# Kernel optimization log

Hardware: AMD Instinct MI355X
Metric: run time of the kernel (lower is better)

The kernel has to match this reference:

```python
import jax, jax.numpy as jnp
import numpy as np

PUSH_MARGIN = 0.25


def setup_inputs() -> dict:
    key = jax.random.key(0)
    k1, k2 = jax.random.split(key)
    B, H, W, D, K = 8, 512, 512, 32, 64
    embeddings = jax.random.normal(k1, (B, H, W, D), dtype=jnp.float32)
    labels = jax.random.randint(k2, (B, H, W), 0, K, dtype=jnp.int32)
    return {"embeddings": embeddings, "labels": labels, "n_instances": K}


def _metric_loss(embeddings, labels, n_instances):
    # embeddings: (B, H, W, D) float; labels: (B, H, W) int; n_instances: static int K
    B = embeddings.shape[0]
    D = embeddings.shape[-1]
    K = n_instances
    emb = embeddings.reshape(B, -1, D)          # (B, N, D)
    lab = labels.reshape(B, -1).astype(jnp.int32)  # (B, N)

    # One-pass segment reduce over all batches: offset labels per batch element.
    seg = (lab + jnp.arange(B, dtype=jnp.int32)[:, None] * K).reshape(-1)  # (B*N,)
    sums = jax.ops.segment_sum(emb.reshape(-1, D), seg, num_segments=B * K)
    counts = jax.ops.segment_sum(jnp.ones(seg.shape, dtype=emb.dtype), seg,
                                 num_segments=B * K)
    sums = sums.reshape(B, K, D)
    counts = counts.reshape(B, K)
    present = counts > 0.5                       # non-empty instances (B, K)
    centroids = sums / jnp.maximum(counts, 1.0)[..., None]  # (B, K, D); zeros if empty

    # Pairwise Manhattan distances between centroids: (B, K, K)
    dist = jnp.sum(jnp.abs(centroids[:, :, None, :] - centroids[:, None, :, :]), axis=-1)
    hinge = jax.nn.relu(PUSH_MARGIN - dist)      # push: relu(margin - d)
    sq = hinge * hinge                           # squared error metric

    # strictly upper triangular + only pairs of non-empty instances
    triu = jnp.triu(jnp.ones((K, K), dtype=bool), k=1)
    pair_mask = triu[None] & present[:, :, None] & present[:, None, :]
    per_image_sum = jnp.sum(jnp.where(pair_mask, sq, 0.0), axis=(1, 2))  # (B,)

    n = jnp.sum(present.astype(emb.dtype), axis=1)              # (B,) non-empty count
    n_comparisons = n * (n - 1.0) / 2.0
    push_loss = per_image_sum / n_comparisons
    return jnp.mean(push_loss)


def reference(embeddings, labels, n_instances):
    return _metric_loss(embeddings, labels, n_instances)
```

## Files before the change

kernel.cpp:

```cpp
#include <hip/hip_runtime.h>

#define B_    8
#define N_    (512 * 512)
#define D_    32
#define K_    64
#define TPB   256
#define NWAVE (TPB / 64)
#define KROW  36
#define TABW  (K_ * KROW)
#define REC   (K_ * D_ + K_)
#define RECQ  (REC / 4)

#define PROC(LB, V, PBASE)                                                    \
  {                                                                           \
    const int    lbc = LB;                                                    \
    const float4 vc  = V;                                                     \
    const int    pb  = (PBASE);                                               \
    if (pb < iend) {                                      \
      LB = lab[bbase + pb + eg];                                              \
      V  = embv[(bbase + pb + eg) * 8 + d4];                                  \
    }                                                                         \
    claimv[lbc] = egl;                           \
    const int win = (claimv[lbc] == egl);             \
    if (d4 == 0) atomicAdd(&cnt[lbc], 1.0f);            \
    const int a = lbc * KROW + d4 * 4;                                        \
    if (win) {                                                                \
      float4 cur = *reinterpret_cast<const float4*>(tab + a);                 \
      cur.x += vc.x; cur.y += vc.y; cur.z += vc.z; cur.w += vc.w;             \
      *reinterpret_cast<float4*>(tab + a) = cur;                              \
    } else {         \
      atomicAdd(&tab[a + 0], vc.x);                                           \
      atomicAdd(&tab[a + 1], vc.y);                                           \
      atomicAdd(&tab[a + 2], vc.z);                                           \
      atomicAdd(&tab[a + 3], vc.w);                                           \
    }                                                                         \
  }

__global__ __launch_bounds__(TPB) void seg_partial_kernel(
    const float* __restrict__ emb, const int* __restrict__ lab,
    float* __restrict__ partials, int blk_per_b)
{
    __shared__ __align__(16) float s_tab[NWAVE * TABW];
    __shared__ float s_cnt[NWAVE * K_];
    __shared__ int   s_claim[NWAVE * K_];

    for (int i = threadIdx.x; i < NWAVE * TABW; i += TPB) s_tab[i] = 0.f;
    for (int i = threadIdx.x; i < NWAVE * K_;  i += TPB) s_cnt[i] = 0.f;
    __syncthreads();

    const int tid  = threadIdx.x;
    const int wave = tid >> 6;
    const int lane = tid & 63;
    const int egl  = lane >> 3;
    const int d4   = lane & 7;
    const int eg   = wave * 8 + egl;

    float* __restrict__ tab = s_tab + wave * TABW;
    float* __restrict__ cnt = s_cnt + wave * K_;
    volatile int* claimv = s_claim + wave * K_;

    const int blk = blockIdx.x;
    const int b   = blk / blk_per_b;
    const int bib = blk - b * blk_per_b;
    const long long bbase = (long long)b * N_;
    const float4* __restrict__ embv = reinterpret_cast<const float4*>(emb);
    const int CHUNK = N_ / blk_per_b;
    int ib = bib * CHUNK;
    const int iend = ib + CHUNK;

    int lbA = lab[bbase + ib + eg];
    float4 vA = embv[(bbase + ib + eg) * 8 + d4];
    int lbB = 0;
    float4 vB = make_float4(0.f, 0.f, 0.f, 0.f);
    if (ib + 32 < iend) {
        lbB = lab[bbase + ib + 32 + eg];
        vB  = embv[(bbase + ib + 32 + eg) * 8 + d4];
    }

    for (;;) {
        PROC(lbA, vA, ib + 64);
        ib += 32;
        if (ib >= iend) break;
        PROC(lbB, vB, ib + 64);
        ib += 32;
        if (ib >= iend) break;
    }
    __syncthreads();

    float* out = partials + (size_t)blk * REC;
    for (int i = tid; i < K_ * D_; i += TPB) {
        int k = i >> 5, d = i & 31;
        float s = 0.f;
#pragma unroll
        for (int w = 0; w < NWAVE; ++w) s += s_tab[w * TABW + k * KROW + d];
        out[i] = s;
    }
    if (tid < K_) {
        float c = 0.f;
#pragma unroll
        for (int w = 0; w < NWAVE; ++w) c += s_cnt[w * K_ + tid];
        out[K_ * D_ + tid] = c;
    }
}

__global__ __launch_bounds__(TPB) void seg_reduce_a(
    const float* __restrict__ partials, float* __restrict__ part2,
    int rpc, int nch)
{
    const int blk = blockIdx.x;
    const int b   = blk / nch;
    const int ch  = blk - b * nch;
    const int tid = threadIdx.x;

    const float4* __restrict__ p4 = reinterpret_cast<const float4*>(partials)
        + (size_t)((b * nch + ch) * rpc) * RECQ;
    float4* __restrict__ o4 = reinterpret_cast<float4*>(part2)
        + (size_t)blk * RECQ;

    float4 acc0 = make_float4(0.f, 0.f, 0.f, 0.f);
    float4 acc1 = acc0, acc2 = acc0;
#pragma unroll 4
    for (int r = 0; r < rpc; ++r) {
        const float4* rp = p4 + (size_t)r * RECQ;
        float4 v0 = rp[tid];
        float4 v1 = rp[tid + 256];
        acc0.x += v0.x; acc0.y += v0.y; acc0.z += v0.z; acc0.w += v0.w;
        acc1.x += v1.x; acc1.y += v1.y; acc1.z += v1.z; acc1.w += v1.w;
        if (tid < 16) {
            float4 v2 = rp[tid + 512];
            acc2.x += v2.x; acc2.y += v2.y; acc2.z += v2.z; acc2.w += v2.w;
        }
    }
    o4[tid]       = acc0;
    o4[tid + 256] = acc1;
    if (tid < 16) o4[tid + 512] = acc2;
}

__global__ __launch_bounds__(TPB) void loss8_kernel(
    const float* __restrict__ part2, float* __restrict__ batch_loss,
    int nch)
{
    __shared__ __align__(16) float4 s_cent4[8 * K_];
    __shared__ float s_cntsh[K_];
    __shared__ float s_pres[K_];
    __shared__ float s_wred[NWAVE];

    const int b   = blockIdx.x;
    const int tid = threadIdx.x;
    const float4* __restrict__ p4 = reinterpret_cast<const float4*>(part2)
        + (size_t)(b * nch) * RECQ;

    float4 acc0 = make_float4(0.f, 0.f, 0.f, 0.f);
    float4 acc1 = acc0, acc2 = acc0;
#pragma unroll 8
    for (int c = 0; c < nch; ++c) {
        const float4* rp = p4 + (size_t)c * RECQ;
        float4 v0 = rp[tid];
        float4 v1 = rp[tid + 256];
        acc0.x += v0.x; acc0.y += v0.y; acc0.z += v0.z; acc0.w += v0.w;
        acc1.x += v1.x; acc1.y += v1.y; acc1.z += v1.z; acc1.w += v1.w;
        if (tid < 16) {
            float4 v2 = rp[tid + 512];
            acc2.x += v2.x; acc2.y += v2.y; acc2.z += v2.z; acc2.w += v2.w;
        }
    }

    s_cent4[(tid & 7) * K_ + (tid >> 3)] = acc0;
    {
        const int q1 = tid + 256;
        s_cent4[(q1 & 7) * K_ + (q1 >> 3)] = acc1;
    }
    if (tid < 16) reinterpret_cast<float4*>(s_cntsh)[tid] = acc2;
    __syncthreads();

    if (tid < K_) s_pres[tid] = (s_cntsh[tid] > 0.5f) ? 1.f : 0.f;
    for (int i = tid; i < 8 * K_; i += TPB) {
        float inv = 1.0f / fmaxf(s_cntsh[i & 63], 1.0f);
        float4 c = s_cent4[i];
        c.x *= inv; c.y *= inv; c.z *= inv; c.w *= inv;
        s_cent4[i] = c;
    }
    __syncthreads();

    const int wave = tid >> 6, lane = tid & 63;

    float4 cb[8];
#pragma unroll
    for (int j = 0; j < 8; ++j) cb[j] = s_cent4[j * K_ + lane];
    const float pres2 = s_pres[lane];

    float acc = 0.f;
#pragma unroll 4
    for (int t = 0; t < 16; ++t) {
        const int k1 = wave * 16 + t;
        float dist = 0.f;
#pragma unroll
        for (int j = 0; j < 8; ++j) {
            float4 a = s_cent4[j * K_ + k1];
            dist += fabsf(a.x - cb[j].x) + fabsf(a.y - cb[j].y)
                  + fabsf(a.z - cb[j].z) + fabsf(a.w - cb[j].w);
        }
        float h = fmaxf(0.25f - dist, 0.f);
        float valid = (k1 < lane) ? s_pres[k1] * pres2 : 0.f;
        acc += valid * h * h;
    }
#pragma unroll
    for (int m = 32; m > 0; m >>= 1) acc += __shfl_xor(acc, m);
    if (lane == 0) s_wred[wave] = acc;
    __syncthreads();
    if (tid == 0) {
        float s = s_wred[0] + s_wred[1] + s_wred[2] + s_wred[3];
        float n = 0.f;
        for (int k = 0; k < K_; ++k) n += s_pres[k];
        float ncomp = n * (n - 1.f) * 0.5f;
        batch_loss[b] = (ncomp > 0.f) ? (s / ncomp) : 0.f;
    }
}

__global__ void final_kernel(const float* __restrict__ batch_loss,
                             float* __restrict__ out)
{
    if (threadIdx.x == 0) {
        float t = 0.f;
#pragma unroll
        for (int b = 0; b < B_; ++b) t += batch_loss[b];
        out[0] = t * (1.0f / (float)B_);
    }
}

extern "C" void kernel_launch(void* const* d_in, const int* in_sizes, int n_in,
                              void* d_out, int out_size, void* d_ws, size_t ws_size,
                              hipStream_t stream)
{
    const float* emb = (const float*)d_in[0];
    const int*   lab = (const int*)d_in[1];
    float*       out = (float*)d_out;
    float*       ws  = (float*)d_ws;

    int blk_per_b = 128;
    while (blk_per_b > 8) {
        size_t need = ((size_t)(blk_per_b * B_) * REC
                       + (size_t)(B_ * 8) * REC
                       + B_) * sizeof(float);
        if (need <= ws_size) break;
        blk_per_b >>= 1;
    }
    const int nblk = blk_per_b * B_;
    const int nch  = (blk_per_b >= 8) ? 8 : blk_per_b;
    const int rpc  = blk_per_b / nch;

    float* partials   = ws;
    float* part2      = ws + (size_t)nblk * REC;
    float* batch_loss = part2 + (size_t)(B_ * nch) * REC;

    seg_partial_kernel<<<nblk, TPB, 0, stream>>>(emb, lab, partials, blk_per_b);

    seg_reduce_a<<<B_ * nch, TPB, 0, stream>>>(partials, part2, rpc, nch);

    loss8_kernel<<<B_, TPB, 0, stream>>>(part2, batch_loss, nch);

    final_kernel<<<1, 64, 0, stream>>>(batch_loss, out);
}
```

Baseline: 81.05 us.

## Detect label collisions in registers and prefetch LDS table rows ahead

Drops the volatile LDS claim array used to choose which lane may do a plain read-modify-write. Each wave now loads its 8 labels as uniform values and builds winner bits with a 64-bit occupancy mask in registers: the first occurrence of a label writes non-atomically and later duplicates use atomics. The main loop runs a fixed trip count and reads the next group's LDS row one step ahead, overlapping that read with the current update and the global prefetch. In exchange it adds scalar bit-manipulation per group and relies on LDS ordering within a wave for the early read to see prior writes.

```diff
diff --git a/kernel.cpp b/kernel.cpp
--- a/kernel.cpp
+++ b/kernel.cpp
@@ -11,29 +11,51 @@
 #define REC   (K_ * D_ + K_)
 #define RECQ  (REC / 4)
 
-#define PROC(LB, V, PBASE)                                                    \
+
+#define PACKNEXT(LBN, WNN, AN)                                                \
   {                                                                           \
-    const int    lbc = LB;                                                    \
-    const float4 vc  = V;                                                     \
-    const int    pb  = (PBASE);                                               \
-    if (pb < iend) {                                      \
-      LB = lab[bbase + pb + eg];                                              \
-      V  = embv[(bbase + pb + eg) * 8 + d4];                                  \
+    unsigned long long occ = 1ull << tn0;                                     \
+    unsigned wbits = 1u;                                                      \
+    unsigned long long bt;                                                    \
+    bt = 1ull << tn1; wbits |= ((occ & bt) ? 0u : 2u);   occ |= bt;           \
+    bt = 1ull << tn2; wbits |= ((occ & bt) ? 0u : 4u);   occ |= bt;           \
+    bt = 1ull << tn3; wbits |= ((occ & bt) ? 0u : 8u);   occ |= bt;           \
+    bt = 1ull << tn4; wbits |= ((occ & bt) ? 0u : 16u);  occ |= bt;           \
+    bt = 1ull << tn5; wbits |= ((occ & bt) ? 0u : 32u);  occ |= bt;           \
+    bt = 1ull << tn6; wbits |= ((occ & bt) ? 0u : 64u);  occ |= bt;           \
+    bt = 1ull << tn7; wbits |= ((occ & bt) ? 0u : 128u);                      \
+    const unsigned plo = (unsigned)tn0 | ((unsigned)tn1 << 8) |               \
+                         ((unsigned)tn2 << 16) | ((unsigned)tn3 << 24);       \
+    const unsigned phi = (unsigned)tn4 | ((unsigned)tn5 << 8) |               \
+                         ((unsigned)tn6 << 16) | ((unsigned)tn7 << 24);       \
+    const unsigned lbsel = lohalf ? plo : phi;                                \
+    LBN = (int)((lbsel >> sh8) & 63u);                                        \
+    WNN = (int)((wbits >> egl) & 1u);                                         \
+    AN  = LBN * KROW + d4x4;                                                  \
+  }
+
+#define BODY(AA, RR, VV, LBX, WNX, AN, RN, LBN, WNN, LOADOK)                  \
+  {                                                                           \
+    if (WNX) {                                                                \
+      float4 cur;                                                             \
+      cur.x = RR.x + VV.x; cur.y = RR.y + VV.y;                               \
+      cur.z = RR.z + VV.z; cur.w = RR.w + VV.w;                               \
+      *reinterpret_cast<float4*>(tab + AA) = cur;                             \
+    } else {         \
+      atomicAdd(&tab[AA + 0], VV.x);                                          \
+      atomicAdd(&tab[AA + 1], VV.y);                                          \
+      atomicAdd(&tab[AA + 2], VV.z);                                          \
+      atomicAdd(&tab[AA + 3], VV.w);                                          \
     }                                                                         \
-    claimv[lbc] = egl;                           \
-    const int win = (claimv[lbc] == egl);             \
-    if (d4 == 0) atomicAdd(&cnt[lbc], 1.0f);            \
-    const int a = lbc * KROW + d4 * 4;                                        \
-    if (win) {                                                                \
-      float4 cur = *reinterpret_cast<const float4*>(tab + a);                 \
-      cur.x += vc.x; cur.y += vc.y; cur.z += vc.z; cur.w += vc.w;             \
-      *reinterpret_cast<float4*>(tab + a) = cur;                              \
-    } else {         \
-      atomicAdd(&tab[a + 0], vc.x);                                           \
-      atomicAdd(&tab[a + 1], vc.y);                                           \
-      atomicAdd(&tab[a + 2], vc.z);                                           \
-      atomicAdd(&tab[a + 3], vc.w);                                           \
+    if (d4 == 0) atomicAdd(&cnt[LBX], 1.0f);         \
+    PACKNEXT(LBN, WNN, AN);                            \
+    if (LOADOK) {                                \
+      tn0 = lpU[0]; tn1 = lpU[1]; tn2 = lpU[2]; tn3 = lpU[3];                 \
+      tn4 = lpU[4]; tn5 = lpU[5]; tn6 = lpU[6]; tn7 = lpU[7];                 \
+      VV  = pe[0];                                                            \
     }                                                                         \
+    lpU += 32; pe += 256;                                                     \
+    RN = *reinterpret_cast<const float4*>(tab + AN);          \
   }
 
 __global__ __launch_bounds__(TPB) void seg_partial_kernel(
@@ -42,7 +64,6 @@
 {
     __shared__ __align__(16) float s_tab[NWAVE * TABW];
     __shared__ float s_cnt[NWAVE * K_];
-    __shared__ int   s_claim[NWAVE * K_];
 
     for (int i = threadIdx.x; i < NWAVE * TABW; i += TPB) s_tab[i] = 0.f;
     for (int i = threadIdx.x; i < NWAVE * K_;  i += TPB) s_cnt[i] = 0.f;
@@ -54,10 +75,12 @@
     const int egl  = lane >> 3;
     const int d4   = lane & 7;
     const int eg   = wave * 8 + egl;
+    const int  d4x4   = d4 * 4;
+    const int  sh8    = (egl & 3) * 8;
+    const bool lohalf = (egl < 4);
 
     float* __restrict__ tab = s_tab + wave * TABW;
     float* __restrict__ cnt = s_cnt + wave * K_;
-    volatile int* claimv = s_claim + wave * K_;
 
     const int blk = blockIdx.x;
     const int b   = blk / blk_per_b;
@@ -65,25 +88,35 @@
     const long long bbase = (long long)b * N_;
     const float4* __restrict__ embv = reinterpret_cast<const float4*>(emb);
     const int CHUNK = N_ / blk_per_b;
-    int ib = bib * CHUNK;
-    const int iend = ib + CHUNK;
-
-    int lbA = lab[bbase + ib + eg];
-    float4 vA = embv[(bbase + ib + eg) * 8 + d4];
-    int lbB = 0;
-    float4 vB = make_float4(0.f, 0.f, 0.f, 0.f);
-    if (ib + 32 < iend) {
-        lbB = lab[bbase + ib + 32 + eg];
-        vB  = embv[(bbase + ib + 32 + eg) * 8 + d4];
-    }
-
-    for (;;) {
-        PROC(lbA, vA, ib + 64);
-        ib += 32;
-        if (ib >= iend) break;
-        PROC(lbB, vB, ib + 64);
-        ib += 32;
-        if (ib >= iend) break;
+    const int NIT   = CHUNK / 32;
+    const int cstart = bib * CHUNK;
+    const int wb = __builtin_amdgcn_readfirstlane(wave * 8);
+
+    const int*    lpU = lab + bbase + cstart + wb;
+    const float4* pe  = embv + (bbase + cstart + eg) * 8 + d4;
+
+    int tn0, tn1, tn2, tn3, tn4, tn5, tn6, tn7;
+    tn0 = lpU[0]; tn1 = lpU[1]; tn2 = lpU[2]; tn3 = lpU[3];
+    tn4 = lpU[4]; tn5 = lpU[5]; tn6 = lpU[6]; tn7 = lpU[7];
+
+    int lbA, wnA, aA, lbB, wnB, aB;
+    PACKNEXT(lbA, wnA, aA);
+
+    float4 vA = pe[0];
+    float4 vB = pe[256];
+
+    tn0 = lpU[32]; tn1 = lpU[33]; tn2 = lpU[34]; tn3 = lpU[35];
+    tn4 = lpU[36]; tn5 = lpU[37]; tn6 = lpU[38]; tn7 = lpU[39];
+
+    lpU += 64;
+    pe  += 512;
+
+    float4 rA = *reinterpret_cast<const float4*>(tab + aA);
+    float4 rB = make_float4(0.f, 0.f, 0.f, 0.f);
+
+    for (int it = 0; it < NIT; it += 2) {
+        BODY(aA, rA, vA, lbA, wnA, aB, rB, lbB, wnB, (it + 2 < NIT));
+        BODY(aB, rB, vB, lbB, wnB, aA, rA, lbA, wnA, (it + 3 < NIT));
     }
     __syncthreads();
 
```

Result: faster. 79.37 us (-2.1%).
